# Optimization experiments

Measured on AMD Instinct MI355X. Metric: run time of the kernel, lower is better.

The kernel has to match this reference:

```python
import jax, jax.numpy as jnp
import numpy as np

B_GRAPHS, N_NODES = 16, 4096
IN_CH, HID = 256, 512
HEADS, HC = 1, 512  # SGFormerAttention(hidden, heads=1, head_channels=hidden)
NUM_LAYERS = 2
LN_EPS = 1e-5
QK_EPS = 1e-6


def setup_inputs() -> dict:
    key = jax.random.key(0)
    ks = jax.random.split(key, 10)

    def w(k, shape, scale=0.02):
        return jax.random.normal(k, shape, jnp.float32) * scale

    inp = {
        "x": jax.random.normal(ks[0], (B_GRAPHS * N_NODES, IN_CH), jnp.float32),
        "fc0_w": w(ks[1], (HID, IN_CH)),
        "fc0_b": jnp.zeros((HID,), jnp.float32),
        "ln0_g": jnp.ones((HID,), jnp.float32),
        "ln0_b": jnp.zeros((HID,), jnp.float32),
        "q0_w": w(ks[2], (HEADS * HC, HID)),
        "k0_w": w(ks[3], (HEADS * HC, HID)),
        "v0_w": w(ks[4], (HEADS * HC, HID)),
        "ln1_g": jnp.ones((HID,), jnp.float32),
        "ln1_b": jnp.zeros((HID,), jnp.float32),
        "q1_w": w(ks[5], (HEADS * HC, HID)),
        "k1_w": w(ks[6], (HEADS * HC, HID)),
        "v1_w": w(ks[7], (HEADS * HC, HID)),
        "ln2_g": jnp.ones((HID,), jnp.float32),
        "ln2_b": jnp.zeros((HID,), jnp.float32),
        "batch": jnp.repeat(jnp.arange(B_GRAPHS, dtype=jnp.int32), N_NODES),
        "num_graphs": B_GRAPHS,
    }
    return inp


def layernorm(x, g, b):
    mu = x.mean(axis=-1, keepdims=True)
    var = ((x - mu) ** 2).mean(axis=-1, keepdims=True)
    return (x - mu) / jnp.sqrt(var + LN_EPS) * g + b


def sg_attention(x, qw, kw, vw):
    # x: [B, N, HID]; linear (kernelized) global attention, softmax-free.
    B, N, _ = x.shape
    q = (x @ qw.T).reshape(B, N, HEADS, HC)
    k = (x @ kw.T).reshape(B, N, HEADS, HC)
    v = (x @ vw.T).reshape(B, N, HEADS, HC)
    q = jnp.where(q == 0, QK_EPS, q)
    k = jnp.where(k == 0, QK_EPS, k)
    q = q / jnp.linalg.norm(q, axis=-1, keepdims=True)
    k = k / jnp.linalg.norm(k, axis=-1, keepdims=True)
    kvs = jnp.einsum('blhm,blhd->bhmd', k, v)          # [B,H,HC,HC]
    num = jnp.einsum('bnhm,bhmd->bnhd', q, kvs) + N * v
    ks_sum = k.sum(axis=1)                             # [B,H,HC]
    denom = jnp.einsum('bnhm,bhm->bnh', q, ks_sum)[..., None] + float(N)
    return (num / denom).mean(axis=2)                  # [B,N,HC] (mean over heads)


def reference(x, fc0_w, fc0_b, ln0_g, ln0_b,
              q0_w, k0_w, v0_w, ln1_g, ln1_b,
              q1_w, k1_w, v1_w, ln2_g, ln2_b,
              batch, num_graphs):
    total = x.shape[0]
    # stable sort by graph id, remember inverse permutation
    indices = jnp.argsort(batch, stable=True)
    rev_perm = jnp.zeros((total,), jnp.int32).at[indices].set(
        jnp.arange(total, dtype=jnp.int32))
    xs = x[indices]
    # uniform graph sizes -> to_dense_batch is a reshape; mask is all-True
    h = xs.reshape(num_graphs, total // num_graphs, x.shape[1])
    h = h @ fc0_w.T + fc0_b
    h = jax.nn.relu(layernorm(h, ln0_g, ln0_b))  # dropout inactive (eval)
    layers = [h]
    for (qw, kw, vw, g, b) in ((q0_w, k0_w, v0_w, ln1_g, ln1_b),
                               (q1_w, k1_w, v1_w, ln2_g, ln2_b)):
        a = sg_attention(layers[-1], qw, kw, vw)
        a = (a + layers[-1]) / 2.0
        a = jax.nn.relu(layernorm(a, g, b))
        layers.append(a)
    out = layers[-1].reshape(total, -1)
    return out[rev_perm]
```

## Files before the change

kernel.cpp:

```cpp
#include <hip/hip_runtime.h>

#define TNODES 65536
#define NGRAPH 16
#define NNODE  4096
#define INCH   256
#define HID    512

using u16 = unsigned short;
using u32 = unsigned int;
using v8s = __attribute__((ext_vector_type(8))) short;
using v4f = __attribute__((ext_vector_type(4))) float;

__device__ __forceinline__ float bf2f(u16 u) {
    union { u32 i; float f; } v; v.i = ((u32)u) << 16; return v.f;
}
__device__ __forceinline__ u16 f2bf(float f) {
    union { float f; u32 i; } v; v.f = f;
    u32 x = v.i;
    return (u16)((x + 0x7fffu + ((x >> 16) & 1u)) >> 16);
}
__device__ __forceinline__ void up4(uint2 p, float* f) {
    f[0] = __uint_as_float(p.x << 16); f[1] = __uint_as_float(p.x & 0xffff0000u);
    f[2] = __uint_as_float(p.y << 16); f[3] = __uint_as_float(p.y & 0xffff0000u);
}
__device__ __forceinline__ uint2 pk4(float a, float b, float c, float d) {
    uint2 r;
    r.x = (u32)f2bf(a) | ((u32)f2bf(b) << 16);
    r.y = (u32)f2bf(c) | ((u32)f2bf(d) << 16);
    return r;
}

#define MFMA(a, b, c) __builtin_amdgcn_mfma_f32_16x16x32_bf16((a), (b), (c), 0, 0, 0)

#define GLD16(gp, sp) __builtin_amdgcn_global_load_lds( \
    (const __attribute__((address_space(1))) u32*)(const void*)(gp), \
    (__attribute__((address_space(3))) u32*)(void*)(sp), 16, 0, 0)

#define CFENCE() asm volatile("" ::: "memory")

__global__ void k_cvt4(const float* __restrict__ s, u16* __restrict__ d, int n4) {
    for (int i = blockIdx.x * blockDim.x + threadIdx.x; i < n4; i += gridDim.x * blockDim.x) {
        float4 f = ((const float4*)s)[i];
        ((uint2*)d)[i] = pk4(f.x, f.y, f.z, f.w);
    }
}

__global__ void k_zero(float* __restrict__ p, int n) {
    int i = blockIdx.x * 256 + threadIdx.x;
    if (i < n) p[i] = 0.f;
}

__global__ void k_red4(const u16* __restrict__ p, u16* __restrict__ o, int n8) {
    const size_t P = (size_t)NGRAPH * HID * HID;
    for (int i = blockIdx.x * blockDim.x + threadIdx.x; i < n8; i += gridDim.x * blockDim.x) {
        size_t b = (size_t)i * 8;
        float s[8] = {0.f, 0.f, 0.f, 0.f, 0.f, 0.f, 0.f, 0.f};
        #pragma unroll
        for (int ss = 0; ss < 4; ++ss) {
            v8s v = *(const v8s*)(p + ss * P + b);
            const u16* vp = (const u16*)&v;
            #pragma unroll
            for (int j = 0; j < 8; ++j) s[j] += bf2f(vp[j]);
        }
        uint2 lo = pk4(s[0], s[1], s[2], s[3]);
        uint2 hi = pk4(s[4], s[5], s[6], s[7]);
        uint4 w; w.x = lo.x; w.y = lo.y; w.z = hi.x; w.w = hi.y;
        *(uint4*)(o + b) = w;
    }
}

template<int LDK, int KLEN>
__device__ __forceinline__ void gemm_core(const u16* __restrict__ A,
                                          const u16* __restrict__ W,
                                          u16* sA, u16* sW, v4f (&acc)[8][4]) {
    const int t = threadIdx.x, lane = t & 63;
    const int q = lane >> 4, m15 = lane & 15;
    const int w = t >> 6, wr = w >> 2, wc = w & 3;

    #pragma unroll
    for (int n = 0; n < 8; ++n)
        #pragma unroll
        for (int rt = 0; rt < 4; ++rt)
            #pragma unroll
            for (int e = 0; e < 4; ++e) acc[n][rt][e] = 0.f;

    int aoff[4], woff[8];
    #pragma unroll
    for (int rt = 0; rt < 4; ++rt) {
        int r = wr * 64 + rt * 16 + m15;
        aoff[rt] = r * 32 + ((q ^ ((r >> 1) & 3)) * 8);
    }
    #pragma unroll
    for (int n = 0; n < 8; ++n) {
        int r = wc * 128 + n * 16 + m15;
        woff[n] = r * 32 + ((q ^ ((r >> 1) & 3)) * 8);
    }

    auto stage = [&](int k0, int buf) {
        u16* dW = sW + buf * (512 * 32);
        #pragma unroll
        for (int p = 0; p < 4; ++p) {
            int sf = p * 512 + t, row = sf >> 2, sl = sf & 3;
            int gc = k0 + ((sl ^ ((row >> 1) & 3)) * 8);
            GLD16(W + (size_t)row * LDK + gc, dW + sf * 8);
        }
        {
            int row = t >> 2, sl = t & 3;
            int gc = k0 + ((sl ^ ((row >> 1) & 3)) * 8);
            GLD16(A + (size_t)row * LDK + gc, sA + buf * (128 * 32) + t * 8);
        }
    };

    const int KT = KLEN / 32;
    stage(0, 0);
    stage(32, 1);
    int cur = 0;
    for (int kt = 0; kt < KT; ++kt) {
        if (kt + 1 < KT) asm volatile("s_waitcnt vmcnt(5)" ::: "memory");
        else             asm volatile("s_waitcnt vmcnt(0)" ::: "memory");
        __builtin_amdgcn_s_barrier();
        CFENCE();
        __builtin_amdgcn_sched_barrier(0);
        const u16* cA = sA + cur * (128 * 32);
        const u16* cW = sW + cur * (512 * 32);
        v8s b[4];
        #pragma unroll
        for (int rt = 0; rt < 4; ++rt) b[rt] = *(const v8s*)(cA + aoff[rt]);
        #pragma unroll
        for (int n = 0; n < 8; ++n) {
            v8s af = *(const v8s*)(cW + woff[n]);
            #pragma unroll
            for (int rt = 0; rt < 4; ++rt)
                acc[n][rt] = MFMA(af, b[rt], acc[n][rt]);
        }
        CFENCE();
        __builtin_amdgcn_s_barrier();
        CFENCE();
        if (kt + 2 < KT) stage((kt + 2) * 32, cur);
        cur ^= 1;
    }
}


__device__ __forceinline__ int tswz(int c) {
    return (((c >> 2) & 3) << 4) ^ ((c & 3) << 3);
}

#define SMEM_DECL __shared__ char smem[81920]
#define SA ((u16*)smem)
#define SW ((u16*)(smem + 16384))

__launch_bounds__(512, 2)
__global__ void k_fc(const u16* __restrict__ xb, const u16* __restrict__ wb,
                     const float* __restrict__ bias, const float* __restrict__ lg,
                     const float* __restrict__ lb, u16* __restrict__ h) {
    SMEM_DECL;
    float (*redA)[4] = (float(*)[4])smem;
    float (*redB)[4] = (float(*)[4])(smem + 2048);
    float* mu_s = (float*)(smem + 4096);
    float* rs_s = (float*)(smem + 4608);
    const int t = threadIdx.x, lane = t & 63, w = t >> 6;
    const int q = lane >> 4, m15 = lane & 15;
    const int wr = w >> 2, wc = w & 3;
    const int bx = (int)blockIdx.x;
    const int swz = (bx & 7) * ((int)gridDim.x >> 3) + (bx >> 3);
    const int r0 = swz * 128;
    v4f acc[8][4];
    gemm_core<INCH, INCH>(xb + (size_t)r0 * INCH, wb, SA, SW, acc);

    float sm[4] = {0.f, 0.f, 0.f, 0.f}, sq[4] = {0.f, 0.f, 0.f, 0.f};
    #pragma unroll
    for (int n = 0; n < 8; ++n) {
        int c = wc * 128 + n * 16 + q * 4;
        float4 bi = *(const float4*)(bias + c);
        const float* bp = &bi.x;
        #pragma unroll
        for (int rt = 0; rt < 4; ++rt)
            #pragma unroll
            for (int e = 0; e < 4; ++e) {
                float a = acc[n][rt][e] + bp[e];
                acc[n][rt][e] = a;
                sm[rt] += a; sq[rt] += a * a;
            }
    }
    #pragma unroll
    for (int rt = 0; rt < 4; ++rt) {
        sm[rt] += __shfl_xor(sm[rt], 16); sm[rt] += __shfl_xor(sm[rt], 32);
        sq[rt] += __shfl_xor(sq[rt], 16); sq[rt] += __shfl_xor(sq[rt], 32);
    }
    if (lane < 16)
        #pragma unroll
        for (int rt = 0; rt < 4; ++rt) {
            redA[wr * 64 + rt * 16 + m15][wc] = sm[rt];
            redB[wr * 64 + rt * 16 + m15][wc] = sq[rt];
        }
    __syncthreads();
    if (t < 128) {
        float tt = redA[t][0] + redA[t][1] + redA[t][2] + redA[t][3];
        float t2 = redB[t][0] + redB[t][1] + redB[t][2] + redB[t][3];
        float mu = tt * (1.f / HID);
        float rs = rsqrtf(t2 * (1.f / HID) - mu * mu + 1e-5f);
        mu_s[t] = mu; rs_s[t] = rs;
    }
    __syncthreads();
    #pragma unroll
    for (int n = 0; n < 8; ++n) {
        int c = wc * 128 + n * 16 + q * 4;
        float4 g4 = *(const float4*)(lg + c);
        float4 b4 = *(const float4*)(lb + c);
        #pragma unroll
        for (int rt = 0; rt < 4; ++rt) {
            int row = wr * 64 + rt * 16 + m15;
            float mu = mu_s[row], rs = rs_s[row];
            float v0 = (acc[n][rt][0] - mu) * rs * g4.x + b4.x;
            float v1 = (acc[n][rt][1] - mu) * rs * g4.y + b4.y;
            float v2 = (acc[n][rt][2] - mu) * rs * g4.z + b4.z;
            float v3 = (acc[n][rt][3] - mu) * rs * g4.w + b4.w;
            v0 = v0 > 0.f ? v0 : 0.f; v1 = v1 > 0.f ? v1 : 0.f;
            v2 = v2 > 0.f ? v2 : 0.f; v3 = v3 > 0.f ? v3 : 0.f;
            *(uint2*)&h[(size_t)(r0 + row) * HID + c] = pk4(v0, v1, v2, v3);
        }
    }
}

__launch_bounds__(512, 2)
__global__ void k_proj(const u16* __restrict__ hsrc, const u16* __restrict__ wkb,
                       const u16* __restrict__ wvb, u16* __restrict__ kt,
                       u16* __restrict__ vt, float* __restrict__ ksum) {
    SMEM_DECL;
    float (*red)[4] = (float(*)[4])smem;
    float* rowv = (float*)(smem + 2048);
    u16* sT = SW;
    const int t = threadIdx.x, lane = t & 63, w = t >> 6;
    const int q = lane >> 4, m15 = lane & 15;
    const int wr = w >> 2, wc = w & 3;
    const int bx = (int)blockIdx.x;
    const int swz = (bx & 7) * ((int)gridDim.x >> 3) + (bx >> 3);
    const int r0 = swz * 128;
    const int g = swz >> 5;
    const int lbase = (swz & 31) * 128;
    const int mode = blockIdx.y;
    v4f acc[8][4];
    gemm_core<HID, HID>(hsrc + (size_t)r0 * HID, mode ? wvb : wkb, SA, SW, acc);

    const int ch = t;
    const int xs = (((ch >> 2) & 3) << 1) ^ (ch & 3);
    if (mode == 0) {
        float sq[4] = {0.f, 0.f, 0.f, 0.f};
        #pragma unroll
        for (int n = 0; n < 8; ++n)
            #pragma unroll
            for (int rt = 0; rt < 4; ++rt)
                #pragma unroll
                for (int e = 0; e < 4; ++e) {
                    float vv = acc[n][rt][e];
                    if (vv == 0.f) vv = 1e-6f;
                    acc[n][rt][e] = vv;
                    sq[rt] += vv * vv;
                }
        #pragma unroll
        for (int rt = 0; rt < 4; ++rt) {
            sq[rt] += __shfl_xor(sq[rt], 16); sq[rt] += __shfl_xor(sq[rt], 32);
        }
        if (lane < 16)
            #pragma unroll
            for (int rt = 0; rt < 4; ++rt)
                red[wr * 64 + rt * 16 + m15][wc] = sq[rt];
        __syncthreads();
        if (t < 128)
            rowv[t] = rsqrtf(red[t][0] + red[t][1] + red[t][2] + red[t][3]);
        __syncthreads();
        float sum = 0.f;
        #pragma unroll
        for (int pass = 0; pass < 2; ++pass) {
            if (wr == pass) {
                #pragma unroll
                for (int n = 0; n < 8; ++n)
                    #pragma unroll
                    for (int rt = 0; rt < 4; ++rt) {
                        int rl = rt * 16 + m15;
                        float rn = rowv[wr * 64 + rl];
                        #pragma unroll
                        for (int e = 0; e < 4; ++e) {
                            int c = wc * 128 + n * 16 + q * 4 + e;
                            sT[(c << 6) + (rl ^ tswz(c))] = f2bf(acc[n][rt][e] * rn);
                        }
                    }
            }
            __syncthreads();
            u16* op = kt + ((size_t)(g * 512 + ch)) * NNODE + lbase + pass * 64;
            #pragma unroll
            for (int jj = 0; jj < 8; ++jj) {
                v8s cvec = *(const v8s*)&sT[(ch << 6) + jj * 8];
                int l0 = (jj ^ xs) * 8;
                *(v8s*)(op + l0) = cvec;
                const u16* cp = (const u16*)&cvec;
                #pragma unroll
                for (int i = 0; i < 8; ++i) sum += bf2f(cp[i]);
            }
            __syncthreads();
        }
        atomicAdd(&ksum[g * 512 + ch], sum);
    } else {
        #pragma unroll
        for (int pass = 0; pass < 2; ++pass) {
            if (wr == pass) {
                #pragma unroll
                for (int n = 0; n < 8; ++n)
                    #pragma unroll
                    for (int rt = 0; rt < 4; ++rt) {
                        int rl = rt * 16 + m15;
                        #pragma unroll
                        for (int e = 0; e < 4; ++e) {
                            int c = wc * 128 + n * 16 + q * 4 + e;
                            sT[(c << 6) + (rl ^ tswz(c))] = f2bf(acc[n][rt][e]);
                        }
                    }
            }
            __syncthreads();
            u16* op = vt + ((size_t)(g * 512 + ch)) * NNODE + lbase + pass * 64;
            #pragma unroll
            for (int jj = 0; jj < 8; ++jj) {
                v8s cvec = *(const v8s*)&sT[(ch << 6) + jj * 8];
                int l0 = (jj ^ xs) * 8;
                *(v8s*)(op + l0) = cvec;
            }
            __syncthreads();
        }
    }
}

__launch_bounds__(512, 2)
__global__ void k_kvmm2(const u16* __restrict__ kt, const u16* __restrict__ vt,
                        u16* __restrict__ kvp) {
    SMEM_DECL;
    const int t = threadIdx.x, lane = t & 63, w = t >> 6;
    const int q = lane >> 4, m15 = lane & 15;
    const int wr = w >> 2, wc = w & 3;
    const int bx = (int)blockIdx.x;
    const int swz = (bx & 7) * 32 + (bx >> 3);
    const int db = swz & 3, s = (swz >> 2) & 3, g = swz >> 4;
    const u16* A = vt + ((size_t)(g * 512 + db * 128)) * NNODE + s * 1024;
    const u16* W = kt + ((size_t)(g * 512)) * NNODE + s * 1024;
    v4f acc[8][4];
    gemm_core<NNODE, 1024>(A, W, SA, SW, acc);
    u16* plane = kvp + (size_t)s * NGRAPH * HID * HID;
    #pragma unroll
    for (int n = 0; n < 8; ++n) {
        int m = wc * 128 + n * 16 + q * 4;
        #pragma unroll
        for (int rt = 0; rt < 4; ++rt) {
            int d = db * 128 + wr * 64 + rt * 16 + m15;
            *(uint2*)&plane[((size_t)(g * 512) + d) * 512 + m] =
                pk4(acc[n][rt][0], acc[n][rt][1], acc[n][rt][2], acc[n][rt][3]);
        }
    }
}

__launch_bounds__(512, 2)
__global__ void k_qnorm(const u16* __restrict__ hsrc, const u16* __restrict__ qwb,
                        const float* __restrict__ ks, u16* __restrict__ qo,
                        float* __restrict__ dnv) {
    SMEM_DECL;
    float (*redA)[4] = (float(*)[4])smem;
    float (*redB)[4] = (float(*)[4])(smem + 2048);
    float* rowv = (float*)(smem + 4096);
    const int t = threadIdx.x, lane = t & 63, w = t >> 6;
    const int q = lane >> 4, m15 = lane & 15;
    const int wr = w >> 2, wc = w & 3;
    const int bx = (int)blockIdx.x;
    const int swz = (bx & 7) * ((int)gridDim.x >> 3) + (bx >> 3);
    const int r0 = swz * 128;
    const int gi = swz >> 5;
    v4f acc[8][4];
    gemm_core<HID, HID>(hsrc + (size_t)r0 * HID, qwb, SA, SW, acc);

    float ss[4] = {0.f, 0.f, 0.f, 0.f}, ws[4] = {0.f, 0.f, 0.f, 0.f};
    #pragma unroll
    for (int n = 0; n < 8; ++n) {
        int c = wc * 128 + n * 16 + q * 4;
        float4 kv = *(const float4*)(ks + (gi << 9) + c);
        const float* kp = &kv.x;
        #pragma unroll
        for (int rt = 0; rt < 4; ++rt)
            #pragma unroll
            for (int e = 0; e < 4; ++e) {
                float vv = acc[n][rt][e];
                if (vv == 0.f) vv = 1e-6f;
                acc[n][rt][e] = vv;
                ss[rt] += vv * vv; ws[rt] += vv * kp[e];
            }
    }
    #pragma unroll
    for (int rt = 0; rt < 4; ++rt) {
        ss[rt] += __shfl_xor(ss[rt], 16); ss[rt] += __shfl_xor(ss[rt], 32);
        ws[rt] += __shfl_xor(ws[rt], 16); ws[rt] += __shfl_xor(ws[rt], 32);
    }
    if (lane < 16)
        #pragma unroll
        for (int rt = 0; rt < 4; ++rt) {
            redA[wr * 64 + rt * 16 + m15][wc] = ss[rt];
            redB[wr * 64 + rt * 16 + m15][wc] = ws[rt];
        }
    __syncthreads();
    if (t < 128) {
        float st = redA[t][0] + redA[t][1] + redA[t][2] + redA[t][3];
        float wt = redB[t][0] + redB[t][1] + redB[t][2] + redB[t][3];
        float rn = rsqrtf(st);
        rowv[t] = rn;
        dnv[r0 + t] = 1.f / (rn * wt + (float)NNODE);
    }
    __syncthreads();
    #pragma unroll
    for (int n = 0; n < 8; ++n) {
        int c = wc * 128 + n * 16 + q * 4;
        #pragma unroll
        for (int rt = 0; rt < 4; ++rt) {
            int row = wr * 64 + rt * 16 + m15;
            float rn = rowv[row];
            *(uint2*)&qo[(size_t)(r0 + row) * HID + c] =
                pk4(acc[n][rt][0] * rn, acc[n][rt][1] * rn,
                    acc[n][rt][2] * rn, acc[n][rt][3] * rn);
        }
    }
}

__launch_bounds__(512, 2)
__global__ void k_attn2(const u16* __restrict__ qhat, const u16* __restrict__ kvstb,
                        const float* __restrict__ dnv, const u16* __restrict__ vt,
                        const u16* __restrict__ hsrc, const float* __restrict__ lg,
                        const float* __restrict__ lb, u16* __restrict__ outb,
                        float* __restrict__ outf) {
    SMEM_DECL;
    float (*redA)[4] = (float(*)[4])smem;
    float (*redB)[4] = (float(*)[4])(smem + 2048);
    float* mu_s = (float*)(smem + 4096);
    float* rs_s = (float*)(smem + 4608);
    const int t = threadIdx.x, lane = t & 63, w = t >> 6;
    const int q = lane >> 4, m15 = lane & 15;
    const int wr = w >> 2, wc = w & 3;
    const int bx = (int)blockIdx.x;
    const int swz = (bx & 7) * ((int)gridDim.x >> 3) + (bx >> 3);
    const int r0 = swz * 128;
    const int gi = swz >> 5;
    v4f acc[8][4];
    gemm_core<HID, HID>(qhat + (size_t)r0 * HID, kvstb + (size_t)gi * HID * HID,
                        SA, SW, acc);

    float dv[4];
    #pragma unroll
    for (int rt = 0; rt < 4; ++rt) dv[rt] = dnv[r0 + wr * 64 + rt * 16 + m15];
    const u16* vtg = vt + (size_t)(gi * 512) * NNODE + ((swz & 31) * 128 + wr * 64 + m15);
    float sm[4] = {0.f, 0.f, 0.f, 0.f}, sq[4] = {0.f, 0.f, 0.f, 0.f};
    #pragma unroll
    for (int n = 0; n < 8; ++n) {
        int c = wc * 128 + n * 16 + q * 4;
        const u16* vb = vtg + (size_t)c * NNODE;
        #pragma unroll
        for (int rt = 0; rt < 4; ++rt) {
            int row = wr * 64 + rt * 16 + m15;
            size_t og = (size_t)(r0 + row) * HID + c;
            float hh[4]; up4(*(const uint2*)&hsrc[og], hh);
            #pragma unroll
            for (int e = 0; e < 4; ++e) {
                float vv = bf2f(vb[(size_t)e * NNODE + rt * 16]);
                float a = ((acc[n][rt][e] + (float)NNODE * vv) * dv[rt] + hh[e]) * 0.5f;
                acc[n][rt][e] = a;
                sm[rt] += a; sq[rt] += a * a;
            }
        }
    }
    #pragma unroll
    for (int rt = 0; rt < 4; ++rt) {
        sm[rt] += __shfl_xor(sm[rt], 16); sm[rt] += __shfl_xor(sm[rt], 32);
        sq[rt] += __shfl_xor(sq[rt], 16); sq[rt] += __shfl_xor(sq[rt], 32);
    }
    if (lane < 16)
        #pragma unroll
        for (int rt = 0; rt < 4; ++rt) {
            redA[wr * 64 + rt * 16 + m15][wc] = sm[rt];
            redB[wr * 64 + rt * 16 + m15][wc] = sq[rt];
        }
    __syncthreads();
    if (t < 128) {
        float tt = redA[t][0] + redA[t][1] + redA[t][2] + redA[t][3];
        float t2 = redB[t][0] + redB[t][1] + redB[t][2] + redB[t][3];
        float mu = tt * (1.f / HID);
        float rs = rsqrtf(t2 * (1.f / HID) - mu * mu + 1e-5f);
        mu_s[t] = mu; rs_s[t] = rs;
    }
    __syncthreads();
    #pragma unroll
    for (int n = 0; n < 8; ++n) {
        int c = wc * 128 + n * 16 + q * 4;
        float4 g4 = *(const float4*)(lg + c);
        float4 b4 = *(const float4*)(lb + c);
        #pragma unroll
        for (int rt = 0; rt < 4; ++rt) {
            int row = wr * 64 + rt * 16 + m15;
            float mu = mu_s[row], rs = rs_s[row];
            float v0 = (acc[n][rt][0] - mu) * rs * g4.x + b4.x;
            float v1 = (acc[n][rt][1] - mu) * rs * g4.y + b4.y;
            float v2 = (acc[n][rt][2] - mu) * rs * g4.z + b4.z;
            float v3 = (acc[n][rt][3] - mu) * rs * g4.w + b4.w;
            v0 = v0 > 0.f ? v0 : 0.f; v1 = v1 > 0.f ? v1 : 0.f;
            v2 = v2 > 0.f ? v2 : 0.f; v3 = v3 > 0.f ? v3 : 0.f;
            size_t og = (size_t)(r0 + row) * HID + c;
            if (outf) {
                float4 o = {v0, v1, v2, v3};
                *(float4*)&outf[og] = o;
            } else {
                *(uint2*)&outb[og] = pk4(v0, v1, v2, v3);
            }
        }
    }
}

extern "C" void kernel_launch(void* const* d_in, const int* in_sizes, int n_in,
                              void* d_out, int out_size, void* d_ws, size_t ws_size,
                              hipStream_t stream) {
    const float* x    = (const float*)d_in[0];
    const float* fc0w = (const float*)d_in[1];
    const float* fc0b = (const float*)d_in[2];
    const float* ln0g = (const float*)d_in[3];
    const float* ln0b = (const float*)d_in[4];
    const float* q0w  = (const float*)d_in[5];
    const float* k0w  = (const float*)d_in[6];
    const float* v0w  = (const float*)d_in[7];
    const float* ln1g = (const float*)d_in[8];
    const float* ln1b = (const float*)d_in[9];
    const float* q1w  = (const float*)d_in[10];
    const float* k1w  = (const float*)d_in[11];
    const float* v1w  = (const float*)d_in[12];
    const float* ln2g = (const float*)d_in[13];
    const float* ln2b = (const float*)d_in[14];

    const size_t M64 = (size_t)TNODES * HID * 2;
    const size_t PL  = (size_t)NGRAPH * HID * HID * 2;
    char* wsc = (char*)d_ws;
    u16*   H   = (u16*)wsc;
    u16*   Kt  = (u16*)(wsc + M64);
    u16*   Vt  = (u16*)(wsc + 2 * M64);
    u16*   KVp = (u16*)(wsc + 3 * M64);
    u16*   KVb = (u16*)(wsc + 3 * M64 + 4 * PL);
    float* KS  = (float*)(wsc + 3 * M64 + 5 * PL);
    float* DNV = KS + NGRAPH * HID;
    u16*   Wc  = (u16*)((char*)DNV + (size_t)TNODES * sizeof(float));
    u16* fc0wb = Wc;
    u16* q0b = Wc + 131072;
    u16* k0b = Wc + 393216;
    u16* v0b = Wc + 655360;
    u16* q1b = Wc + 917504;
    u16* k1b = Wc + 1179648;
    u16* v1b = Wc + 1441792;
    u16* Xb  = Vt;
    u16* QH  = Kt;

    dim3 b256(256), b512(512);
    k_cvt4<<<dim3(64),  b256, 0, stream>>>(fc0w, fc0wb, HID * INCH / 4);
    k_cvt4<<<dim3(64),  b256, 0, stream>>>(q0w, q0b, HID * HID / 4);
    k_cvt4<<<dim3(64),  b256, 0, stream>>>(k0w, k0b, HID * HID / 4);
    k_cvt4<<<dim3(64),  b256, 0, stream>>>(v0w, v0b, HID * HID / 4);
    k_cvt4<<<dim3(64),  b256, 0, stream>>>(q1w, q1b, HID * HID / 4);
    k_cvt4<<<dim3(64),  b256, 0, stream>>>(k1w, k1b, HID * HID / 4);
    k_cvt4<<<dim3(64),  b256, 0, stream>>>(v1w, v1b, HID * HID / 4);
    k_cvt4<<<dim3(1024), b256, 0, stream>>>(x, Xb, TNODES * INCH / 4);

    k_fc<<<dim3(TNODES / 128), b512, 0, stream>>>(Xb, fc0wb, fc0b, ln0g, ln0b, H);

    k_zero<<<dim3(32), b256, 0, stream>>>(KS, NGRAPH * HID);
    k_proj<<<dim3(TNODES / 128, 2), b512, 0, stream>>>(H, k0b, v0b, Kt, Vt, KS);
    k_kvmm2<<<dim3(256), b512, 0, stream>>>(Kt, Vt, KVp);
    k_red4<<<dim3(2048), b256, 0, stream>>>(KVp, KVb, NGRAPH * HID * HID / 8);
    k_qnorm<<<dim3(TNODES / 128), b512, 0, stream>>>(H, q0b, KS, QH, DNV);
    k_attn2<<<dim3(TNODES / 128), b512, 0, stream>>>(QH, KVb, DNV, Vt, H, ln1g, ln1b,
                                                     H, nullptr);

    k_zero<<<dim3(32), b256, 0, stream>>>(KS, NGRAPH * HID);
    k_proj<<<dim3(TNODES / 128, 2), b512, 0, stream>>>(H, k1b, v1b, Kt, Vt, KS);
    k_kvmm2<<<dim3(256), b512, 0, stream>>>(Kt, Vt, KVp);
    k_red4<<<dim3(2048), b256, 0, stream>>>(KVp, KVb, NGRAPH * HID * HID / 8);
    k_qnorm<<<dim3(TNODES / 128), b512, 0, stream>>>(H, q1b, KS, QH, DNV);
    k_attn2<<<dim3(TNODES / 128), b512, 0, stream>>>(QH, KVb, DNV, Vt, H, ln2g, ln2b,
                                                     nullptr, (float*)d_out);
}
```

Measured before the change: 909.7 us.

## Load A operand fragments directly from global into registers, dropping LDS staging

The shared GEMM core no longer stages the 128-row A tile through LDS. Each wave reads its own A fragments straight from global memory into double-buffered registers, two k-steps ahead, while W still goes through the LDS double buffer. This removes the A-tile LDS writes and reads and shrinks shared memory from 80KB to about 70KB. In exchange there are more outstanding global loads per thread, A fragments are no longer shared across the four column-waves (so A is re-read four times from cache), and register pressure rises.

```diff
diff --git a/kernel.cpp b/kernel.cpp
--- a/kernel.cpp
+++ b/kernel.cpp
@@ -72,7 +72,7 @@
 template<int LDK, int KLEN>
 __device__ __forceinline__ void gemm_core(const u16* __restrict__ A,
                                           const u16* __restrict__ W,
-                                          u16* sA, u16* sW, v4f (&acc)[8][4]) {
+                                          u16* sW, v4f (&acc)[8][4]) {
     const int t = threadIdx.x, lane = t & 63;
     const int q = lane >> 4, m15 = lane & 15;
     const int w = t >> 6, wr = w >> 2, wc = w & 3;
@@ -84,19 +84,18 @@
             #pragma unroll
             for (int e = 0; e < 4; ++e) acc[n][rt][e] = 0.f;
 
-    int aoff[4], woff[8];
-    #pragma unroll
-    for (int rt = 0; rt < 4; ++rt) {
-        int r = wr * 64 + rt * 16 + m15;
-        aoff[rt] = r * 32 + ((q ^ ((r >> 1) & 3)) * 8);
-    }
+    int woff[8];
     #pragma unroll
     for (int n = 0; n < 8; ++n) {
         int r = wc * 128 + n * 16 + m15;
         woff[n] = r * 32 + ((q ^ ((r >> 1) & 3)) * 8);
     }
-
-    auto stage = [&](int k0, int buf) {
+    const u16* aptr[4];
+    #pragma unroll
+    for (int rt = 0; rt < 4; ++rt)
+        aptr[rt] = A + (size_t)(wr * 64 + rt * 16 + m15) * LDK + q * 8;
+
+    auto stageW = [&](int k0, int buf) {
         u16* dW = sW + buf * (512 * 32);
         #pragma unroll
         for (int p = 0; p < 4; ++p) {
@@ -104,41 +103,49 @@
             int gc = k0 + ((sl ^ ((row >> 1) & 3)) * 8);
             GLD16(W + (size_t)row * LDK + gc, dW + sf * 8);
         }
-        {
-            int row = t >> 2, sl = t & 3;
-            int gc = k0 + ((sl ^ ((row >> 1) & 3)) * 8);
-            GLD16(A + (size_t)row * LDK + gc, sA + buf * (128 * 32) + t * 8);
-        }
     };
 
     const int KT = KLEN / 32;
-    stage(0, 0);
-    stage(32, 1);
-    int cur = 0;
-    for (int kt = 0; kt < KT; ++kt) {
-        if (kt + 1 < KT) asm volatile("s_waitcnt vmcnt(5)" ::: "memory");
-        else             asm volatile("s_waitcnt vmcnt(0)" ::: "memory");
-        __builtin_amdgcn_s_barrier();
-        CFENCE();
-        __builtin_amdgcn_sched_barrier(0);
-        const u16* cA = sA + cur * (128 * 32);
-        const u16* cW = sW + cur * (512 * 32);
-        v8s b[4];
-        #pragma unroll
-        for (int rt = 0; rt < 4; ++rt) b[rt] = *(const v8s*)(cA + aoff[rt]);
-        #pragma unroll
-        for (int n = 0; n < 8; ++n) {
-            v8s af = *(const v8s*)(cW + woff[n]);
-            #pragma unroll
-            for (int rt = 0; rt < 4; ++rt)
-                acc[n][rt] = MFMA(af, b[rt], acc[n][rt]);
-        }
-        CFENCE();
-        __builtin_amdgcn_s_barrier();
-        CFENCE();
-        if (kt + 2 < KT) stage((kt + 2) * 32, cur);
-        cur ^= 1;
-    }
+    v8s arA[4], arB[4];
+    stageW(0, 0);
+    #pragma unroll
+    for (int rt = 0; rt < 4; ++rt) arA[rt] = *(const v8s*)(aptr[rt]);
+    stageW(32, 1);
+    #pragma unroll
+    for (int rt = 0; rt < 4; ++rt) arB[rt] = *(const v8s*)(aptr[rt] + 32);
+
+    #define GSTEP(KTI, AR, BUF)                                              \
+    {                                                                        \
+        if ((KTI) + 1 < KT) asm volatile("s_waitcnt vmcnt(8)" ::: "memory"); \
+        else                asm volatile("s_waitcnt vmcnt(0)" ::: "memory"); \
+        __builtin_amdgcn_s_barrier();                                        \
+        CFENCE();                                                            \
+        __builtin_amdgcn_sched_barrier(0);                                   \
+        const u16* cW = sW + (BUF) * (512 * 32);                             \
+        _Pragma("unroll")                                                    \
+        for (int n = 0; n < 8; ++n) {                                        \
+            v8s af = *(const v8s*)(cW + woff[n]);                            \
+            _Pragma("unroll")                                                \
+            for (int rt = 0; rt < 4; ++rt)                                   \
+                acc[n][rt] = MFMA(af, AR[rt], acc[n][rt]);                   \
+        }                                                                    \
+        CFENCE();                                                            \
+        if ((KTI) + 2 < KT) {                                                \
+            _Pragma("unroll")                                                \
+            for (int rt = 0; rt < 4; ++rt)                                   \
+                AR[rt] = *(const v8s*)(aptr[rt] + ((KTI) + 2) * 32);         \
+        }                                                                    \
+        CFENCE();                                                            \
+        __builtin_amdgcn_s_barrier();                                        \
+        CFENCE();                                                            \
+        if ((KTI) + 2 < KT) stageW(((KTI) + 2) * 32, (BUF));                 \
+    }
+
+    for (int kt = 0; kt < KT; kt += 2) {
+        GSTEP(kt, arA, 0)
+        GSTEP(kt + 1, arB, 1)
+    }
+    #undef GSTEP
 }
 
 
@@ -146,19 +153,19 @@
     return (((c >> 2) & 3) << 4) ^ ((c & 3) << 3);
 }
 
-#define SMEM_DECL __shared__ char smem[81920]
-#define SA ((u16*)smem)
-#define SW ((u16*)(smem + 16384))
+#define SMEM_DECL __shared__ char smem[65536 + 6144]
+#define SW ((u16*)smem)
+#define EPI (smem + 65536)
 
 __launch_bounds__(512, 2)
 __global__ void k_fc(const u16* __restrict__ xb, const u16* __restrict__ wb,
                      const float* __restrict__ bias, const float* __restrict__ lg,
                      const float* __restrict__ lb, u16* __restrict__ h) {
     SMEM_DECL;
-    float (*redA)[4] = (float(*)[4])smem;
-    float (*redB)[4] = (float(*)[4])(smem + 2048);
-    float* mu_s = (float*)(smem + 4096);
-    float* rs_s = (float*)(smem + 4608);
+    float (*redA)[4] = (float(*)[4])EPI;
+    float (*redB)[4] = (float(*)[4])(EPI + 2048);
+    float* mu_s = (float*)(EPI + 4096);
+    float* rs_s = (float*)(EPI + 4608);
     const int t = threadIdx.x, lane = t & 63, w = t >> 6;
     const int q = lane >> 4, m15 = lane & 15;
     const int wr = w >> 2, wc = w & 3;
@@ -166,7 +173,7 @@
     const int swz = (bx & 7) * ((int)gridDim.x >> 3) + (bx >> 3);
     const int r0 = swz * 128;
     v4f acc[8][4];
-    gemm_core<INCH, INCH>(xb + (size_t)r0 * INCH, wb, SA, SW, acc);
+    gemm_core<INCH, INCH>(xb + (size_t)r0 * INCH, wb, SW, acc);
 
     float sm[4] = {0.f, 0.f, 0.f, 0.f}, sq[4] = {0.f, 0.f, 0.f, 0.f};
     #pragma unroll
@@ -228,8 +235,8 @@
                        const u16* __restrict__ wvb, u16* __restrict__ kt,
                        u16* __restrict__ vt, float* __restrict__ ksum) {
     SMEM_DECL;
-    float (*red)[4] = (float(*)[4])smem;
-    float* rowv = (float*)(smem + 2048);
+    float (*red)[4] = (float(*)[4])EPI;
+    float* rowv = (float*)(EPI + 2048);
     u16* sT = SW;
     const int t = threadIdx.x, lane = t & 63, w = t >> 6;
     const int q = lane >> 4, m15 = lane & 15;
@@ -241,7 +248,7 @@
     const int lbase = (swz & 31) * 128;
     const int mode = blockIdx.y;
     v4f acc[8][4];
-    gemm_core<HID, HID>(hsrc + (size_t)r0 * HID, mode ? wvb : wkb, SA, SW, acc);
+    gemm_core<HID, HID>(hsrc + (size_t)r0 * HID, mode ? wvb : wkb, SW, acc);
 
     const int ch = t;
     const int xs = (((ch >> 2) & 3) << 1) ^ (ch & 3);
@@ -343,7 +350,7 @@
     const u16* A = vt + ((size_t)(g * 512 + db * 128)) * NNODE + s * 1024;
     const u16* W = kt + ((size_t)(g * 512)) * NNODE + s * 1024;
     v4f acc[8][4];
-    gemm_core<NNODE, 1024>(A, W, SA, SW, acc);
+    gemm_core<NNODE, 1024>(A, W, SW, acc);
     u16* plane = kvp + (size_t)s * NGRAPH * HID * HID;
     #pragma unroll
     for (int n = 0; n < 8; ++n) {
@@ -362,9 +369,9 @@
                         const float* __restrict__ ks, u16* __restrict__ qo,
                         float* __restrict__ dnv) {
     SMEM_DECL;
-    float (*redA)[4] = (float(*)[4])smem;
-    float (*redB)[4] = (float(*)[4])(smem + 2048);
-    float* rowv = (float*)(smem + 4096);
+    float (*redA)[4] = (float(*)[4])EPI;
+    float (*redB)[4] = (float(*)[4])(EPI + 2048);
+    float* rowv = (float*)(EPI + 4096);
     const int t = threadIdx.x, lane = t & 63, w = t >> 6;
     const int q = lane >> 4, m15 = lane & 15;
     const int wr = w >> 2, wc = w & 3;
@@ -373,7 +380,7 @@
     const int r0 = swz * 128;
     const int gi = swz >> 5;
     v4f acc[8][4];
-    gemm_core<HID, HID>(hsrc + (size_t)r0 * HID, qwb, SA, SW, acc);
+    gemm_core<HID, HID>(hsrc + (size_t)r0 * HID, qwb, SW, acc);
 
     float ss[4] = {0.f, 0.f, 0.f, 0.f}, ws[4] = {0.f, 0.f, 0.f, 0.f};
     #pragma unroll
@@ -432,10 +439,10 @@
                         const float* __restrict__ lb, u16* __restrict__ outb,
                         float* __restrict__ outf) {
     SMEM_DECL;
-    float (*redA)[4] = (float(*)[4])smem;
-    float (*redB)[4] = (float(*)[4])(smem + 2048);
-    float* mu_s = (float*)(smem + 4096);
-    float* rs_s = (float*)(smem + 4608);
+    float (*redA)[4] = (float(*)[4])EPI;
+    float (*redB)[4] = (float(*)[4])(EPI + 2048);
+    float* mu_s = (float*)(EPI + 4096);
+    float* rs_s = (float*)(EPI + 4608);
     const int t = threadIdx.x, lane = t & 63, w = t >> 6;
     const int q = lane >> 4, m15 = lane & 15;
     const int wr = w >> 2, wc = w & 3;
@@ -445,7 +452,7 @@
     const int gi = swz >> 5;
     v4f acc[8][4];
     gemm_core<HID, HID>(qhat + (size_t)r0 * HID, kvstb + (size_t)gi * HID * HID,
-                        SA, SW, acc);
+                        SW, acc);
 
     float dv[4];
     #pragma unroll
```

Result: slower. 1.080 ms (+18.7%).

## Merge KV outer-product and Q-normalization into one launch, batch weight conversions

Applied to the files above, without the earlier changes.

When the workspace is large enough, Q gets its own buffer instead of sharing Kt, so the kv matmul and the q projection/normalization can run in a single grid. Blocks 0-255 do the kv work and the rest do qnorm, letting the small 256-block kv grid overlap with qnorm and filling the device. The seven weight-conversion launches are also folded into one 2D launch. This costs extra workspace memory and adds a fallback path when the workspace is smaller.

```diff
diff --git a/kernel.cpp b/kernel.cpp
--- a/kernel.cpp
+++ b/kernel.cpp
@@ -39,6 +39,22 @@
 #define CFENCE() asm volatile("" ::: "memory")
 
 __global__ void k_cvt4(const float* __restrict__ s, u16* __restrict__ d, int n4) {
+    for (int i = blockIdx.x * blockDim.x + threadIdx.x; i < n4; i += gridDim.x * blockDim.x) {
+        float4 f = ((const float4*)s)[i];
+        ((uint2*)d)[i] = pk4(f.x, f.y, f.z, f.w);
+    }
+}
+
+struct CvtArgs {
+    const float* s[7];
+    u16* d[7];
+    int n4[7];
+};
+__global__ void k_cvtw(CvtArgs a) {
+    const int y = blockIdx.y;
+    const float* s = a.s[y];
+    u16* d = a.d[y];
+    const int n4 = a.n4[y];
     for (int i = blockIdx.x * blockDim.x + threadIdx.x; i < n4; i += gridDim.x * blockDim.x) {
         float4 f = ((const float4*)s)[i];
         ((uint2*)d)[i] = pk4(f.x, f.y, f.z, f.w);
@@ -330,20 +346,20 @@
     }
 }
 
-__launch_bounds__(512, 2)
-__global__ void k_kvmm2(const u16* __restrict__ kt, const u16* __restrict__ vt,
-                        u16* __restrict__ kvp) {
-    SMEM_DECL;
+__device__ __forceinline__ void kvmm2_body(int bx, char* smemp,
+        const u16* __restrict__ kt, const u16* __restrict__ vt,
+        u16* __restrict__ kvp) {
+    u16* sA = (u16*)smemp;
+    u16* sW = (u16*)(smemp + 16384);
     const int t = threadIdx.x, lane = t & 63, w = t >> 6;
     const int q = lane >> 4, m15 = lane & 15;
     const int wr = w >> 2, wc = w & 3;
-    const int bx = (int)blockIdx.x;
     const int swz = (bx & 7) * 32 + (bx >> 3);
     const int db = swz & 3, s = (swz >> 2) & 3, g = swz >> 4;
     const u16* A = vt + ((size_t)(g * 512 + db * 128)) * NNODE + s * 1024;
     const u16* W = kt + ((size_t)(g * 512)) * NNODE + s * 1024;
     v4f acc[8][4];
-    gemm_core<NNODE, 1024>(A, W, SA, SW, acc);
+    gemm_core<NNODE, 1024>(A, W, sA, sW, acc);
     u16* plane = kvp + (size_t)s * NGRAPH * HID * HID;
     #pragma unroll
     for (int n = 0; n < 8; ++n) {
@@ -357,23 +373,23 @@
     }
 }
 
-__launch_bounds__(512, 2)
-__global__ void k_qnorm(const u16* __restrict__ hsrc, const u16* __restrict__ qwb,
-                        const float* __restrict__ ks, u16* __restrict__ qo,
-                        float* __restrict__ dnv) {
-    SMEM_DECL;
-    float (*redA)[4] = (float(*)[4])smem;
-    float (*redB)[4] = (float(*)[4])(smem + 2048);
-    float* rowv = (float*)(smem + 4096);
+__device__ __forceinline__ void qnorm_body(int bx, char* smemp,
+        const u16* __restrict__ hsrc, const u16* __restrict__ qwb,
+        const float* __restrict__ ks, u16* __restrict__ qo,
+        float* __restrict__ dnv) {
+    u16* sA = (u16*)smemp;
+    u16* sW = (u16*)(smemp + 16384);
+    float (*redA)[4] = (float(*)[4])smemp;
+    float (*redB)[4] = (float(*)[4])(smemp + 2048);
+    float* rowv = (float*)(smemp + 4096);
     const int t = threadIdx.x, lane = t & 63, w = t >> 6;
     const int q = lane >> 4, m15 = lane & 15;
     const int wr = w >> 2, wc = w & 3;
-    const int bx = (int)blockIdx.x;
-    const int swz = (bx & 7) * ((int)gridDim.x >> 3) + (bx >> 3);
+    const int swz = (bx & 7) * 64 + (bx >> 3);
     const int r0 = swz * 128;
     const int gi = swz >> 5;
     v4f acc[8][4];
-    gemm_core<HID, HID>(hsrc + (size_t)r0 * HID, qwb, SA, SW, acc);
+    gemm_core<HID, HID>(hsrc + (size_t)r0 * HID, qwb, sA, sW, acc);
 
     float ss[4] = {0.f, 0.f, 0.f, 0.f}, ws[4] = {0.f, 0.f, 0.f, 0.f};
     #pragma unroll
@@ -423,6 +439,32 @@
                     acc[n][rt][2] * rn, acc[n][rt][3] * rn);
         }
     }
+}
+
+__launch_bounds__(512, 2)
+__global__ void k_kvmm2(const u16* __restrict__ kt, const u16* __restrict__ vt,
+                        u16* __restrict__ kvp) {
+    SMEM_DECL;
+    kvmm2_body((int)blockIdx.x, smem, kt, vt, kvp);
+}
+
+__launch_bounds__(512, 2)
+__global__ void k_qnorm(const u16* __restrict__ hsrc, const u16* __restrict__ qwb,
+                        const float* __restrict__ ks, u16* __restrict__ qo,
+                        float* __restrict__ dnv) {
+    SMEM_DECL;
+    qnorm_body((int)blockIdx.x, smem, hsrc, qwb, ks, qo, dnv);
+}
+
+__launch_bounds__(512, 2)
+__global__ void k_mq(const u16* __restrict__ kt, const u16* __restrict__ vt,
+                     u16* __restrict__ kvp, const u16* __restrict__ hsrc,
+                     const u16* __restrict__ qwb, const float* __restrict__ ks,
+                     u16* __restrict__ qo, float* __restrict__ dnv) {
+    SMEM_DECL;
+    const int bx = (int)blockIdx.x;
+    if (bx < 256) kvmm2_body(bx, smem, kt, vt, kvp);
+    else          qnorm_body(bx - 256, smem, hsrc, qwb, ks, qo, dnv);
 }
 
 __launch_bounds__(512, 2)
@@ -537,15 +579,23 @@
 
     const size_t M64 = (size_t)TNODES * HID * 2;
     const size_t PL  = (size_t)NGRAPH * HID * HID * 2;
-    char* wsc = (char*)d_ws;
-    u16*   H   = (u16*)wsc;
-    u16*   Kt  = (u16*)(wsc + M64);
-    u16*   Vt  = (u16*)(wsc + 2 * M64);
-    u16*   KVp = (u16*)(wsc + 3 * M64);
-    u16*   KVb = (u16*)(wsc + 3 * M64 + 4 * PL);
-    float* KS  = (float*)(wsc + 3 * M64 + 5 * PL);
-    float* DNV = KS + NGRAPH * HID;
-    u16*   Wc  = (u16*)((char*)DNV + (size_t)TNODES * sizeof(float));
+    const size_t KS_SZ  = (size_t)NGRAPH * HID * sizeof(float);
+    const size_t DNV_SZ = (size_t)TNODES * sizeof(float);
+    const size_t WC_SZ  = (size_t)1703936 * 2;
+    const size_t NEED_BIG = 4 * M64 + 5 * PL + KS_SZ + DNV_SZ + WC_SZ;
+    const bool bigws = ws_size >= NEED_BIG;
+
+    char* p = (char*)d_ws;
+    u16*   H   = (u16*)p;  p += M64;
+    u16*   Kt  = (u16*)p;  p += M64;
+    u16*   Vt  = (u16*)p;  p += M64;
+    u16*   QHb = nullptr;
+    if (bigws) { QHb = (u16*)p; p += M64; }
+    u16*   KVp = (u16*)p;  p += 4 * PL;
+    u16*   KVb = (u16*)p;  p += PL;
+    float* KS  = (float*)p; p += KS_SZ;
+    float* DNV = (float*)p; p += DNV_SZ;
+    u16*   Wc  = (u16*)p;
     u16* fc0wb = Wc;
     u16* q0b = Wc + 131072;
     u16* k0b = Wc + 393216;
@@ -554,33 +604,43 @@
     u16* k1b = Wc + 1179648;
     u16* v1b = Wc + 1441792;
     u16* Xb  = Vt;
-    u16* QH  = Kt;
+    u16* QH  = bigws ? QHb : Kt;
 
     dim3 b256(256), b512(512);
-    k_cvt4<<<dim3(64),  b256, 0, stream>>>(fc0w, fc0wb, HID * INCH / 4);
-    k_cvt4<<<dim3(64),  b256, 0, stream>>>(q0w, q0b, HID * HID / 4);
-    k_cvt4<<<dim3(64),  b256, 0, stream>>>(k0w, k0b, HID * HID / 4);
-    k_cvt4<<<dim3(64),  b256, 0, stream>>>(v0w, v0b, HID * HID / 4);
-    k_cvt4<<<dim3(64),  b256, 0, stream>>>(q1w, q1b, HID * HID / 4);
-    k_cvt4<<<dim3(64),  b256, 0, stream>>>(k1w, k1b, HID * HID / 4);
-    k_cvt4<<<dim3(64),  b256, 0, stream>>>(v1w, v1b, HID * HID / 4);
+    CvtArgs ca;
+    ca.s[0] = fc0w; ca.d[0] = fc0wb; ca.n4[0] = HID * INCH / 4;
+    ca.s[1] = q0w;  ca.d[1] = q0b;   ca.n4[1] = HID * HID / 4;
+    ca.s[2] = k0w;  ca.d[2] = k0b;   ca.n4[2] = HID * HID / 4;
+    ca.s[3] = v0w;  ca.d[3] = v0b;   ca.n4[3] = HID * HID / 4;
+    ca.s[4] = q1w;  ca.d[4] = q1b;   ca.n4[4] = HID * HID / 4;
+    ca.s[5] = k1w;  ca.d[5] = k1b;   ca.n4[5] = HID * HID / 4;
+    ca.s[6] = v1w;  ca.d[6] = v1b;   ca.n4[6] = HID * HID / 4;
+    k_cvtw<<<dim3(64, 7), b256, 0, stream>>>(ca);
     k_cvt4<<<dim3(1024), b256, 0, stream>>>(x, Xb, TNODES * INCH / 4);
 
     k_fc<<<dim3(TNODES / 128), b512, 0, stream>>>(Xb, fc0wb, fc0b, ln0g, ln0b, H);
 
     k_zero<<<dim3(32), b256, 0, stream>>>(KS, NGRAPH * HID);
     k_proj<<<dim3(TNODES / 128, 2), b512, 0, stream>>>(H, k0b, v0b, Kt, Vt, KS);
-    k_kvmm2<<<dim3(256), b512, 0, stream>>>(Kt, Vt, KVp);
+    if (bigws) {
+        k_mq<<<dim3(768), b512, 0, stream>>>(Kt, Vt, KVp, H, q0b, KS, QH, DNV);
+    } else {
+        k_kvmm2<<<dim3(256), b512, 0, stream>>>(Kt, Vt, KVp);
+        k_qnorm<<<dim3(512), b512, 0, stream>>>(H, q0b, KS, QH, DNV);
+    }
     k_red4<<<dim3(2048), b256, 0, stream>>>(KVp, KVb, NGRAPH * HID * HID / 8);
-    k_qnorm<<<dim3(TNODES / 128), b512, 0, stream>>>(H, q0b, KS, QH, DNV);
     k_attn2<<<dim3(TNODES / 128), b512, 0, stream>>>(QH, KVb, DNV, Vt, H, ln1g, ln1b,
                                                      H, nullptr);
 
     k_zero<<<dim3(32), b256, 0, stream>>>(KS, NGRAPH * HID);
     k_proj<<<dim3(TNODES / 128, 2), b512, 0, stream>>>(H, k1b, v1b, Kt, Vt, KS);
-    k_kvmm2<<<dim3(256), b512, 0, stream>>>(Kt, Vt, KVp);
+    if (bigws) {
+        k_mq<<<dim3(768), b512, 0, stream>>>(Kt, Vt, KVp, H, q1b, KS, QH, DNV);
+    } else {
+        k_kvmm2<<<dim3(256), b512, 0, stream>>>(Kt, Vt, KVp);
+        k_qnorm<<<dim3(512), b512, 0, stream>>>(H, q1b, KS, QH, DNV);
+    }
     k_red4<<<dim3(2048), b256, 0, stream>>>(KVp, KVb, NGRAPH * HID * HID / 8);
-    k_qnorm<<<dim3(TNODES / 128), b512, 0, stream>>>(H, q1b, KS, QH, DNV);
     k_attn2<<<dim3(TNODES / 128), b512, 0, stream>>>(QH, KVb, DNV, Vt, H, ln2g, ln2b,
                                                      nullptr, (float*)d_out);
 }
```

Result: no change. 899.8 us (-1.1%).
